# Performance work log

Hardware: AMD Instinct MI355X
Metric: run time of the kernel (lower is better)

Reference implementation:

```python
import jax, jax.numpy as jnp
import numpy as np

# Dims: N nodes, 2 CSR scales, hidden H=128, attention A=64, L=3 layers
N = 50000
E0, E1 = 600000, 200000   # edges per scale (avg degree 12 and 4)
H, A, L, S = 128, 64, 3, 2
F, CD = 16, 2             # field channels, coord dim
GEOM = S * (CD + 1)       # geometry embedding dim: mean rel offset + mean dist per scale


def setup_inputs() -> dict:
    key = jax.random.key(0)
    ks = jax.random.split(key, 12)
    coords = jax.random.normal(ks[0], (N, CD), jnp.float32)
    fields = jax.random.normal(ks[1], (N, F), jnp.float32)
    # CSR with fixed degrees (regular indptr, random irregular neighbor indices)
    indptr0 = (jnp.arange(N + 1, dtype=jnp.int32) * (E0 // N)).astype(jnp.int32)
    indices0 = jax.random.randint(ks[2], (E0,), 0, N, dtype=jnp.int32)
    indptr1 = (jnp.arange(N + 1, dtype=jnp.int32) * (E1 // N)).astype(jnp.int32)
    indices1 = jax.random.randint(ks[3], (E1,), 0, N, dtype=jnp.int32)
    # Learned parameters
    W_in = jax.random.normal(ks[4], (F + GEOM, H), jnp.float32) / np.sqrt(F + GEOM)
    b_in = jnp.zeros((H,), jnp.float32)
    Wq = jax.random.normal(ks[5], (L, S, H, A), jnp.float32) / np.sqrt(H)
    Wk = jax.random.normal(ks[6], (L, S, H, A), jnp.float32) / np.sqrt(H)
    Wv = jax.random.normal(ks[7], (L, S, H, H), jnp.float32) / np.sqrt(H)
    Wo = jax.random.normal(ks[8], (L, S * H, H), jnp.float32) / np.sqrt(S * H)
    bo = jnp.zeros((L, H), jnp.float32)
    return {"coords": coords, "fields": fields,
            "indptr0": indptr0, "indices0": indices0,
            "indptr1": indptr1, "indices1": indices1,
            "W_in": W_in, "b_in": b_in, "Wq": Wq, "Wk": Wk, "Wv": Wv,
            "Wo": Wo, "bo": bo}


def _csr_rows(indptr, num_edges):
    deg = indptr[1:] - indptr[:-1]
    return jnp.repeat(jnp.arange(indptr.shape[0] - 1), deg, total_repeat_length=num_edges)


def _geom_scale(coords, rows, cols, indptr):
    # per-node mean relative offset and mean neighbor distance over one scale
    n = indptr.shape[0] - 1
    rel = coords[cols] - coords[rows]                     # [E, CD]
    dist = jnp.linalg.norm(rel, axis=-1, keepdims=True)   # [E, 1]
    deg = (indptr[1:] - indptr[:-1]).astype(coords.dtype)[:, None]
    feats = jnp.concatenate([rel, dist], axis=-1)         # [E, CD+1]
    return jax.ops.segment_sum(feats, rows, num_segments=n) / jnp.maximum(deg, 1.0)


def _segment_softmax(scores, rows, n):
    m = jax.ops.segment_max(scores, rows, num_segments=n)
    ex = jnp.exp(scores - m[rows])
    den = jax.ops.segment_sum(ex, rows, num_segments=n)
    return ex / den[rows]


def reference(coords, fields, indptr0, indices0, indptr1, indices1,
              W_in, b_in, Wq, Wk, Wv, Wo, bo):
    n = coords.shape[0]
    csr = [(indptr0, indices0), (indptr1, indices1)]
    rows = [_csr_rows(ip, ix.shape[0]) for ip, ix in csr]
    # geometry embedding: concat per-scale neighborhood stats -> [N, GEOM]
    geom = jnp.concatenate(
        [_geom_scale(coords, rows[s], csr[s][1], csr[s][0]) for s in range(len(csr))], axis=-1)
    # prologue: concat fields+geom, Dense, gelu (flax gelu is tanh-approx)
    x = jax.nn.gelu(jnp.concatenate([fields, geom], axis=-1) @ W_in + b_in)
    eps = 1e-6
    for l in range(Wq.shape[0]):
        aggs = []
        for s in range(Wq.shape[1]):
            r, c = rows[s], csr[s][1]
            q = x @ Wq[l, s]           # [N, A]
            k = x @ Wk[l, s]           # [N, A]
            v = x @ Wv[l, s]           # [N, H]
            qn = q / (jnp.linalg.norm(q, axis=-1, keepdims=True) + eps)
            kn = k / (jnp.linalg.norm(k, axis=-1, keepdims=True) + eps)
            score = jnp.sum(qn[r] * kn[c], axis=-1)       # cosine attention per edge
            alpha = _segment_softmax(score, r, n)
            aggs.append(jax.ops.segment_sum(alpha[:, None] * v[c], r, num_segments=n))
        x = x + jax.nn.gelu(jnp.concatenate(aggs, axis=-1) @ Wo[l] + bo[l])
    return x
```

## Files before the change

kernel.cpp:

```cpp
#include <hip/hip_runtime.h>
#include <hip/hip_fp16.h>
#include <math.h>

#define HD 128

typedef _Float16 f16x8 __attribute__((ext_vector_type(8)));
typedef float f32x4 __attribute__((ext_vector_type(4)));

__device__ __forceinline__ f16x8 f16x8_zero() {
    f16x8 v = {(_Float16)0, (_Float16)0, (_Float16)0, (_Float16)0,
               (_Float16)0, (_Float16)0, (_Float16)0, (_Float16)0};
    return v;
}

__device__ __forceinline__ float gelu_tanh(float v) {
    float v3 = v * v * v;
    float t = tanhf(0.7978845608028654f * (v + 0.044715f * v3));
    return 0.5f * v * (1.0f + t);
}

__device__ __forceinline__ void store_h4(__half* p, float4 a) {
    __half2 lo = __float22half2_rn(make_float2(a.x, a.y));
    __half2 hi = __float22half2_rn(make_float2(a.z, a.w));
    uint2 u;
    u.x = *(unsigned*)&lo;
    u.y = *(unsigned*)&hi;
    *(uint2*)p = u;
}

__device__ __forceinline__ float4 load_h4(const __half* p) {
    uint2 raw = *(const uint2*)p;
    float2 lo = __half22float2(*(__half2*)&raw.x);
    float2 hi = __half22float2(*(__half2*)&raw.y);
    return make_float4(lo.x, lo.y, hi.x, hi.y);
}

__global__ void convert_wqkv_kernel(const float* __restrict__ Wq,
                                    const float* __restrict__ Wk,
                                    const float* __restrict__ Wv,
                                    __half* __restrict__ Wt) {
    int idx = blockIdx.x * 256 + threadIdx.x;
    if (idx >= 6 * 256 * 32) return;
    int ls = idx / (256 * 32);
    int rem = idx - ls * (256 * 32);
    int oc = rem >> 5;
    int k4 = rem & 31;
    const float* src;
    int stride, col;
    if (oc < 64)       { src = Wq + (size_t)ls * 128 * 64;  stride = 64;  col = oc; }
    else if (oc < 128) { src = Wk + (size_t)ls * 128 * 64;  stride = 64;  col = oc - 64; }
    else               { src = Wv + (size_t)ls * 128 * 128; stride = 128; col = oc - 128; }
    float4 v;
    v.x = src[(k4 * 4 + 0) * stride + col];
    v.y = src[(k4 * 4 + 1) * stride + col];
    v.z = src[(k4 * 4 + 2) * stride + col];
    v.w = src[(k4 * 4 + 3) * stride + col];
    store_h4(&Wt[(size_t)ls * 256 * 128 + (size_t)oc * 128 + k4 * 4], v);
}

__global__ void convert_wo_kernel(const float* __restrict__ Wo,
                                  __half* __restrict__ Wot) {
    int idx = blockIdx.x * 256 + threadIdx.x;
    if (idx >= 3 * 128 * 64) return;
    int l = idx / (128 * 64);
    int rem = idx - l * (128 * 64);
    int oc = rem >> 6;
    int k4 = rem & 63;
    const float* src = Wo + (size_t)l * 256 * 128;
    float4 v;
    v.x = src[(k4 * 4 + 0) * 128 + oc];
    v.y = src[(k4 * 4 + 1) * 128 + oc];
    v.z = src[(k4 * 4 + 2) * 128 + oc];
    v.w = src[(k4 * 4 + 3) * 128 + oc];
    store_h4(&Wot[(size_t)l * 128 * 256 + (size_t)oc * 256 + k4 * 4], v);
}

__global__ void geom_kernel(const float* __restrict__ coords,
                            const int* __restrict__ ip0, const int* __restrict__ ix0,
                            const int* __restrict__ ip1, const int* __restrict__ ix1,
                            float* __restrict__ geom, int n) {
    int i = blockIdx.x * blockDim.x + threadIdx.x;
    if (i >= n) return;
    float cx = coords[2 * i], cy = coords[2 * i + 1];
    #pragma unroll
    for (int s = 0; s < 2; ++s) {
        const int* ip = s ? ip1 : ip0;
        const int* ix = s ? ix1 : ix0;
        int st = ip[i], en = ip[i + 1];
        float sx = 0.f, sy = 0.f, sd = 0.f;
        for (int e = st; e < en; ++e) {
            int c = ix[e];
            float dx = coords[2 * c] - cx;
            float dy = coords[2 * c + 1] - cy;
            sx += dx; sy += dy;
            sd += sqrtf(dx * dx + dy * dy);
        }
        float inv = 1.0f / fmaxf((float)(en - st), 1.0f);
        geom[6 * i + 3 * s + 0] = sx * inv;
        geom[6 * i + 3 * s + 1] = sy * inv;
        geom[6 * i + 3 * s + 2] = sd * inv;
    }
}

__global__ void prologue_kernel(const float* __restrict__ fields,
                                const float* __restrict__ geom,
                                const float* __restrict__ W_in,
                                const float* __restrict__ b_in,
                                float* __restrict__ x,
                                __half* __restrict__ xh, int n) {
    int node = blockIdx.x * 2 + (threadIdx.x >> 7);
    int col = threadIdx.x & 127;
    if (node >= n) return;
    float acc = b_in[col];
    const float* f = fields + (size_t)node * 16;
    const float* g = geom + (size_t)node * 6;
    #pragma unroll
    for (int k = 0; k < 16; ++k) acc += f[k] * W_in[k * HD + col];
    #pragma unroll
    for (int k = 0; k < 6; ++k) acc += g[k] * W_in[(16 + k) * HD + col];
    float r = gelu_tanh(acc);
    x[(size_t)node * HD + col] = r;
    xh[(size_t)node * HD + col] = __float2half(r);
}

__global__ __launch_bounds__(256)
void qkv_mfma_kernel(const __half* __restrict__ xh,
                     const __half* __restrict__ Wt,
                     __half* __restrict__ qh,
                     __half* __restrict__ kh,
                     __half* __restrict__ vh,
                     int n) {
    __shared__ __half Xs[64 * 128];
    int t = threadIdx.x;
    int lane = t & 63, w = t >> 6;
    int m0 = blockIdx.x * 64;

    #pragma unroll
    for (int it = 0; it < 4; ++it) {
        int idx = t + it * 256;
        int row = idx >> 4, slot = idx & 15;
        int sw = slot ^ (row & 7);
        f16x8 v = f16x8_zero();
        if (m0 + row < n)
            v = *(const f16x8*)&xh[(size_t)(m0 + row) * 128 + slot * 8];
        *(f16x8*)&Xs[row * 128 + sw * 8] = v;
    }
    __syncthreads();

    int lr = lane & 15, lq = lane >> 4;
    f32x4 acc[4][4];
    #pragma unroll
    for (int nf = 0; nf < 4; ++nf)
        #pragma unroll
        for (int of = 0; of < 4; ++of) {
            f32x4 z = {0.f, 0.f, 0.f, 0.f};
            acc[nf][of] = z;
        }

    const __half* Wbase = Wt + (size_t)(w * 64) * 128;
    #pragma unroll
    for (int ts = 0; ts < 4; ++ts) {
        int koct = ts * 4 + lq;
        f16x8 wf[4], xf[4];
        #pragma unroll
        for (int of = 0; of < 4; ++of)
            wf[of] = *(const f16x8*)&Wbase[(size_t)(of * 16 + lr) * 128 + koct * 8];
        #pragma unroll
        for (int nf = 0; nf < 4; ++nf) {
            int row = nf * 16 + lr;
            int sw = koct ^ (row & 7);
            xf[nf] = *(const f16x8*)&Xs[row * 128 + sw * 8];
        }
        #pragma unroll
        for (int nf = 0; nf < 4; ++nf)
            #pragma unroll
            for (int of = 0; of < 4; ++of)
                acc[nf][of] = __builtin_amdgcn_mfma_f32_16x16x32_f16(
                    wf[of], xf[nf], acc[nf][of], 0, 0, 0);
    }

    if (w < 2) {
        #pragma unroll
        for (int nf = 0; nf < 4; ++nf) {
            float s = 0.f;
            #pragma unroll
            for (int of = 0; of < 4; ++of) {
                f32x4 a = acc[nf][of];
                s += a[0] * a[0] + a[1] * a[1] + a[2] * a[2] + a[3] * a[3];
            }
            s += __shfl_xor(s, 16, 64);
            s += __shfl_xor(s, 32, 64);
            float f = 1.0f / (sqrtf(s) + 1e-6f);
            #pragma unroll
            for (int of = 0; of < 4; ++of) {
                acc[nf][of][0] *= f; acc[nf][of][1] *= f;
                acc[nf][of][2] *= f; acc[nf][of][3] *= f;
            }
        }
    }

    #pragma unroll
    for (int nf = 0; nf < 4; ++nf) {
        int node = m0 + nf * 16 + lr;
        if (node >= n) continue;
        #pragma unroll
        for (int of = 0; of < 4; ++of) {
            int oc = of * 16 + lq * 4;
            float4 v = make_float4(acc[nf][of][0], acc[nf][of][1],
                                   acc[nf][of][2], acc[nf][of][3]);
            if (w == 0)      store_h4(&qh[(size_t)node * 64 + oc], v);
            else if (w == 1) store_h4(&kh[(size_t)node * 64 + oc], v);
            else if (w == 2) store_h4(&vh[(size_t)node * 128 + oc], v);
            else             store_h4(&vh[(size_t)node * 128 + 64 + oc], v);
        }
    }
}

template<int DEG>
__global__ void attn_kernel_t(const __half* __restrict__ qh,
                              const __half* __restrict__ kh,
                              const __half* __restrict__ vh,
                              const int* __restrict__ indptr,
                              const int* __restrict__ indices,
                              __half* __restrict__ aggh,
                              int scale, int n) {
    int wid = threadIdx.x >> 6;
    int lane = threadIdx.x & 63;
    int i = blockIdx.x * (blockDim.x >> 6) + wid;
    if (i >= n) return;
    int g = lane >> 4, sl = lane & 15;
    int st = indptr[i];

    float4 q = load_h4(&qh[(size_t)i * 64 + sl * 4]);

    float sc[DEG];
    constexpr int NIT = (DEG + 3) / 4;
    #pragma unroll
    for (int it = 0; it < NIT; ++it) {
        int e = it * 4 + g;
        int ee = (e < DEG) ? e : (DEG - 1);
        int c = indices[st + ee];
        float4 k = load_h4(&kh[(size_t)c * 64 + sl * 4]);
        float p = q.x * k.x + q.y * k.y + q.z * k.z + q.w * k.w;
        p += __shfl_xor(p, 1, 64);
        p += __shfl_xor(p, 2, 64);
        p += __shfl_xor(p, 4, 64);
        p += __shfl_xor(p, 8, 64);
        #pragma unroll
        for (int j = 0; j < 4; ++j) {
            int e2 = it * 4 + j;
            if (e2 < DEG) sc[e2] = __shfl(p, j * 16, 64);
        }
    }

    float mx = sc[0];
    #pragma unroll
    for (int e = 1; e < DEG; ++e) mx = fmaxf(mx, sc[e]);
    float den = 0.f;
    #pragma unroll
    for (int e = 0; e < DEG; ++e) { sc[e] = __expf(sc[e] - mx); den += sc[e]; }
    float inv = 1.0f / den;

    int half = lane >> 5, hl = lane & 31;
    float4 a = make_float4(0.f, 0.f, 0.f, 0.f);
    #pragma unroll
    for (int it = 0; it < DEG / 2; ++it) {
        int c = indices[st + 2 * it + half];
        float al = (half ? sc[2 * it + 1] : sc[2 * it]) * inv;
        float4 v = load_h4(&vh[(size_t)c * 128 + hl * 4]);
        a.x += al * v.x; a.y += al * v.y; a.z += al * v.z; a.w += al * v.w;
    }
    a.x += __shfl_xor(a.x, 32, 64);
    a.y += __shfl_xor(a.y, 32, 64);
    a.z += __shfl_xor(a.z, 32, 64);
    a.w += __shfl_xor(a.w, 32, 64);
    if (half == 0)
        store_h4(&aggh[(size_t)i * 256 + scale * 128 + hl * 4], a);
}

__global__ void attn_generic(const __half* __restrict__ qh,
                             const __half* __restrict__ kh,
                             const __half* __restrict__ vh,
                             const int* __restrict__ indptr,
                             const int* __restrict__ indices,
                             __half* __restrict__ aggh, int scale, int n) {
    int wid = threadIdx.x >> 6;
    int lane = threadIdx.x & 63;
    int i = blockIdx.x * (blockDim.x >> 6) + wid;
    if (i >= n) return;
    int g = lane >> 4, sl = lane & 15;
    int st = indptr[i];
    int deg = indptr[i + 1] - st;
    if (deg > 32) deg = 32;
    if (deg <= 0) {
        if (lane < 32)
            store_h4(&aggh[(size_t)i * 256 + scale * 128 + (lane & 31) * 4],
                     make_float4(0.f, 0.f, 0.f, 0.f));
        return;
    }
    float4 q = load_h4(&qh[(size_t)i * 64 + sl * 4]);
    float sc[32];
    for (int e0 = 0; e0 < deg; e0 += 4) {
        int e = e0 + g;
        int ee = (e < deg) ? e : (deg - 1);
        int c = indices[st + ee];
        float4 k = load_h4(&kh[(size_t)c * 64 + sl * 4]);
        float p = q.x * k.x + q.y * k.y + q.z * k.z + q.w * k.w;
        p += __shfl_xor(p, 1, 64);
        p += __shfl_xor(p, 2, 64);
        p += __shfl_xor(p, 4, 64);
        p += __shfl_xor(p, 8, 64);
        for (int j = 0; j < 4; ++j)
            if (e0 + j < deg) sc[e0 + j] = __shfl(p, j * 16, 64);
    }
    float mx = -INFINITY;
    for (int e = 0; e < deg; ++e) mx = fmaxf(mx, sc[e]);
    float den = 0.f;
    for (int e = 0; e < deg; ++e) { sc[e] = __expf(sc[e] - mx); den += sc[e]; }
    float inv = 1.0f / den;
    int half = lane >> 5, hl = lane & 31;
    float4 a = make_float4(0.f, 0.f, 0.f, 0.f);
    for (int e0 = 0; e0 < deg; e0 += 2) {
        int e = e0 + half;
        if (e < deg) {
            int c = indices[st + e];
            float al = sc[e] * inv;
            float4 v = load_h4(&vh[(size_t)c * 128 + hl * 4]);
            a.x += al * v.x; a.y += al * v.y; a.z += al * v.z; a.w += al * v.w;
        }
    }
    a.x += __shfl_xor(a.x, 32, 64);
    a.y += __shfl_xor(a.y, 32, 64);
    a.z += __shfl_xor(a.z, 32, 64);
    a.w += __shfl_xor(a.w, 32, 64);
    if (half == 0)
        store_h4(&aggh[(size_t)i * 256 + scale * 128 + hl * 4], a);
}

__global__ __launch_bounds__(256)
void wo_mfma_kernel(const __half* __restrict__ aggh,
                    const __half* __restrict__ Wot,
                    const float* __restrict__ bo,
                    float* __restrict__ x,
                    __half* __restrict__ xh,
                    int n) {
    __shared__ __half As[64 * 256];
    int t = threadIdx.x;
    int lane = t & 63, w = t >> 6;
    int m0 = blockIdx.x * 64;

    #pragma unroll
    for (int it = 0; it < 8; ++it) {
        int idx = t + it * 256;
        int row = idx >> 5, slot = idx & 31;
        int sw = slot ^ (row & 7);
        f16x8 v = f16x8_zero();
        if (m0 + row < n)
            v = *(const f16x8*)&aggh[(size_t)(m0 + row) * 256 + slot * 8];
        *(f16x8*)&As[row * 256 + sw * 8] = v;
    }
    __syncthreads();

    int lr = lane & 15, lq = lane >> 4;
    f32x4 acc[4][2];
    #pragma unroll
    for (int nf = 0; nf < 4; ++nf)
        #pragma unroll
        for (int of = 0; of < 2; ++of) {
            f32x4 z = {0.f, 0.f, 0.f, 0.f};
            acc[nf][of] = z;
        }

    const __half* Wbase = Wot + (size_t)(w * 32) * 256;
    #pragma unroll
    for (int ts = 0; ts < 8; ++ts) {
        int koct = ts * 4 + lq;
        f16x8 wf[2], af[4];
        #pragma unroll
        for (int of = 0; of < 2; ++of)
            wf[of] = *(const f16x8*)&Wbase[(size_t)(of * 16 + lr) * 256 + koct * 8];
        #pragma unroll
        for (int nf = 0; nf < 4; ++nf) {
            int row = nf * 16 + lr;
            int sw = koct ^ (row & 7);
            af[nf] = *(const f16x8*)&As[row * 256 + sw * 8];
        }
        #pragma unroll
        for (int nf = 0; nf < 4; ++nf)
            #pragma unroll
            for (int of = 0; of < 2; ++of)
                acc[nf][of] = __builtin_amdgcn_mfma_f32_16x16x32_f16(
                    wf[of], af[nf], acc[nf][of], 0, 0, 0);
    }

    #pragma unroll
    for (int nf = 0; nf < 4; ++nf) {
        int node = m0 + nf * 16 + lr;
        if (node >= n) continue;
        #pragma unroll
        for (int of = 0; of < 2; ++of) {
            int oc = w * 32 + of * 16 + lq * 4;
            float4 b = *(const float4*)&bo[oc];
            float4 xv = *(const float4*)&x[(size_t)node * 128 + oc];
            float4 r;
            r.x = xv.x + gelu_tanh(acc[nf][of][0] + b.x);
            r.y = xv.y + gelu_tanh(acc[nf][of][1] + b.y);
            r.z = xv.z + gelu_tanh(acc[nf][of][2] + b.z);
            r.w = xv.w + gelu_tanh(acc[nf][of][3] + b.w);
            *(float4*)&x[(size_t)node * 128 + oc] = r;
            store_h4(&xh[(size_t)node * 128 + oc], r);
        }
    }
}

extern "C" void kernel_launch(void* const* d_in, const int* in_sizes, int n_in,
                              void* d_out, int out_size, void* d_ws, size_t ws_size,
                              hipStream_t stream) {
    const float* coords = (const float*)d_in[0];
    const float* fields = (const float*)d_in[1];
    const int*   ip0    = (const int*)d_in[2];
    const int*   ix0    = (const int*)d_in[3];
    const int*   ip1    = (const int*)d_in[4];
    const int*   ix1    = (const int*)d_in[5];
    const float* W_in   = (const float*)d_in[6];
    const float* b_in   = (const float*)d_in[7];
    const float* Wq     = (const float*)d_in[8];
    const float* Wk     = (const float*)d_in[9];
    const float* Wv     = (const float*)d_in[10];
    const float* Wo     = (const float*)d_in[11];
    const float* bo     = (const float*)d_in[12];

    int n = in_sizes[0] / 2;
    float* x = (float*)d_out;

    char* ws = (char*)d_ws;
    size_t off = 0;
    auto carve = [&](size_t bytes) {
        void* p = ws + off;
        off = (off + bytes + 255) & ~(size_t)255;
        return p;
    };
    float*  geom = (float*)carve((size_t)n * 6 * 4);
    __half* xh   = (__half*)carve((size_t)n * 128 * 2);
    __half* qh   = (__half*)carve((size_t)n * 64 * 2);
    __half* kh   = (__half*)carve((size_t)n * 64 * 2);
    __half* vh   = (__half*)carve((size_t)n * 128 * 2);
    __half* aggh = (__half*)carve((size_t)n * 256 * 2);
    __half* Wt   = (__half*)carve((size_t)6 * 256 * 128 * 2);
    __half* Wot  = (__half*)carve((size_t)3 * 128 * 256 * 2);

    convert_wqkv_kernel<<<(6 * 256 * 32 + 255) / 256, 256, 0, stream>>>(Wq, Wk, Wv, Wt);
    convert_wo_kernel<<<(3 * 128 * 64 + 255) / 256, 256, 0, stream>>>(Wo, Wot);

    geom_kernel<<<(n + 255) / 256, 256, 0, stream>>>(coords, ip0, ix0, ip1, ix1, geom, n);
    prologue_kernel<<<(n + 1) / 2, 256, 0, stream>>>(fields, geom, W_in, b_in, x, xh, n);

    int deg0 = in_sizes[3] / n;
    int deg1 = in_sizes[5] / n;

    auto launch_attn = [&](int deg, const int* ip, const int* ix, int scale) {
        int ab = (n + 3) / 4;
        bool uniform = (deg * n == (scale ? in_sizes[5] : in_sizes[3]));
        if (uniform) {
            switch (deg) {
                case 4:  attn_kernel_t<4><<<ab, 256, 0, stream>>>(qh, kh, vh, ip, ix, aggh, scale, n); return;
                case 6:  attn_kernel_t<6><<<ab, 256, 0, stream>>>(qh, kh, vh, ip, ix, aggh, scale, n); return;
                case 8:  attn_kernel_t<8><<<ab, 256, 0, stream>>>(qh, kh, vh, ip, ix, aggh, scale, n); return;
                case 12: attn_kernel_t<12><<<ab, 256, 0, stream>>>(qh, kh, vh, ip, ix, aggh, scale, n); return;
                case 16: attn_kernel_t<16><<<ab, 256, 0, stream>>>(qh, kh, vh, ip, ix, aggh, scale, n); return;
            }
        }
        attn_generic<<<ab, 256, 0, stream>>>(qh, kh, vh, ip, ix, aggh, scale, n);
    };

    int gblocks = (n + 63) / 64;
    for (int l = 0; l < 3; ++l) {
        for (int s = 0; s < 2; ++s) {
            const __half* wt = Wt + (size_t)(l * 2 + s) * 256 * 128;
            qkv_mfma_kernel<<<gblocks, 256, 0, stream>>>(xh, wt, qh, kh, vh, n);
            launch_attn(s ? deg1 : deg0, s ? ip1 : ip0, s ? ix1 : ix0, s);
        }
        wo_mfma_kernel<<<gblocks, 256, 0, stream>>>(aggh, Wot + (size_t)l * 128 * 256,
                                                    bo + l * 128, x, xh, n);
    }
}
```

Measured before the change: 593.7 us.

## Fuse per-layer QKV for both scales and merge both scales' attention into one kernel

The geometry kernel is folded into the prologue kernel: one thread per node computes the neighbourhood stats into shared memory, and the geom buffer disappears. The QKV projection now computes both scales in a single 512-thread launch that reuses the staged X tile, writing into separate per-scale q/k/v buffers. A dual attention kernel processes both scales, with node/scale items interleaved across waves. Gathers of indices, K and V are batched into registers before use to raise memory-level parallelism. These changes cut kernel launches and the re-reading of x, at the cost of a serialized single-lane geom loop in the prologue and a dual path specialized to degrees 12 and 4.

After: 570.5 us. 1.04x faster.

```diff
diff --git a/kernel.cpp b/kernel.cpp
--- a/kernel.cpp
+++ b/kernel.cpp
@@ -75,69 +75,71 @@
     store_h4(&Wot[(size_t)l * 128 * 256 + (size_t)oc * 256 + k4 * 4], v);
 }
 
-__global__ void geom_kernel(const float* __restrict__ coords,
-                            const int* __restrict__ ip0, const int* __restrict__ ix0,
-                            const int* __restrict__ ip1, const int* __restrict__ ix1,
-                            float* __restrict__ geom, int n) {
-    int i = blockIdx.x * blockDim.x + threadIdx.x;
-    if (i >= n) return;
-    float cx = coords[2 * i], cy = coords[2 * i + 1];
-    #pragma unroll
-    for (int s = 0; s < 2; ++s) {
-        const int* ip = s ? ip1 : ip0;
-        const int* ix = s ? ix1 : ix0;
-        int st = ip[i], en = ip[i + 1];
-        float sx = 0.f, sy = 0.f, sd = 0.f;
-        for (int e = st; e < en; ++e) {
-            int c = ix[e];
-            float dx = coords[2 * c] - cx;
-            float dy = coords[2 * c + 1] - cy;
-            sx += dx; sy += dy;
-            sd += sqrtf(dx * dx + dy * dy);
-        }
-        float inv = 1.0f / fmaxf((float)(en - st), 1.0f);
-        geom[6 * i + 3 * s + 0] = sx * inv;
-        geom[6 * i + 3 * s + 1] = sy * inv;
-        geom[6 * i + 3 * s + 2] = sd * inv;
-    }
-}
-
-__global__ void prologue_kernel(const float* __restrict__ fields,
-                                const float* __restrict__ geom,
-                                const float* __restrict__ W_in,
-                                const float* __restrict__ b_in,
-                                float* __restrict__ x,
-                                __half* __restrict__ xh, int n) {
-    int node = blockIdx.x * 2 + (threadIdx.x >> 7);
+__global__ void geom_prologue_kernel(const float* __restrict__ coords,
+                                     const float* __restrict__ fields,
+                                     const int* __restrict__ ip0, const int* __restrict__ ix0,
+                                     const int* __restrict__ ip1, const int* __restrict__ ix1,
+                                     const float* __restrict__ W_in,
+                                     const float* __restrict__ b_in,
+                                     float* __restrict__ x,
+                                     __half* __restrict__ xh, int n) {
+    __shared__ float gsh[2][6];
+    int slot = threadIdx.x >> 7;
+    int node = blockIdx.x * 2 + slot;
     int col = threadIdx.x & 127;
-    if (node >= n) return;
+    bool valid = node < n;
+
+    if (valid && col == 0) {
+        float cx = coords[2 * node], cy = coords[2 * node + 1];
+        #pragma unroll
+        for (int s = 0; s < 2; ++s) {
+            const int* ip = s ? ip1 : ip0;
+            const int* ix = s ? ix1 : ix0;
+            int st = ip[node], en = ip[node + 1];
+            float sx = 0.f, sy = 0.f, sd = 0.f;
+            for (int e = st; e < en; ++e) {
+                int c = ix[e];
+                float dx = coords[2 * c] - cx;
+                float dy = coords[2 * c + 1] - cy;
+                sx += dx; sy += dy;
+                sd += sqrtf(dx * dx + dy * dy);
+            }
+            float inv = 1.0f / fmaxf((float)(en - st), 1.0f);
+            gsh[slot][3 * s + 0] = sx * inv;
+            gsh[slot][3 * s + 1] = sy * inv;
+            gsh[slot][3 * s + 2] = sd * inv;
+        }
+    }
+    __syncthreads();
+    if (!valid) return;
+
     float acc = b_in[col];
     const float* f = fields + (size_t)node * 16;
-    const float* g = geom + (size_t)node * 6;
     #pragma unroll
     for (int k = 0; k < 16; ++k) acc += f[k] * W_in[k * HD + col];
     #pragma unroll
-    for (int k = 0; k < 6; ++k) acc += g[k] * W_in[(16 + k) * HD + col];
+    for (int k = 0; k < 6; ++k) acc += gsh[slot][k] * W_in[(16 + k) * HD + col];
     float r = gelu_tanh(acc);
     x[(size_t)node * HD + col] = r;
     xh[(size_t)node * HD + col] = __float2half(r);
 }
 
-__global__ __launch_bounds__(256)
-void qkv_mfma_kernel(const __half* __restrict__ xh,
-                     const __half* __restrict__ Wt,
-                     __half* __restrict__ qh,
-                     __half* __restrict__ kh,
-                     __half* __restrict__ vh,
-                     int n) {
+__global__ __launch_bounds__(512)
+void qkv_dual_mfma_kernel(const __half* __restrict__ xh,
+                          const __half* __restrict__ WtL,
+                          __half* __restrict__ qh0, __half* __restrict__ kh0,
+                          __half* __restrict__ vh0,
+                          __half* __restrict__ qh1, __half* __restrict__ kh1,
+                          __half* __restrict__ vh1,
+                          int n) {
     __shared__ __half Xs[64 * 128];
     int t = threadIdx.x;
     int lane = t & 63, w = t >> 6;
     int m0 = blockIdx.x * 64;
 
     #pragma unroll
-    for (int it = 0; it < 4; ++it) {
-        int idx = t + it * 256;
+    for (int it = 0; it < 2; ++it) {
+        int idx = t + it * 512;
         int row = idx >> 4, slot = idx & 15;
         int sw = slot ^ (row & 7);
         f16x8 v = f16x8_zero();
@@ -147,6 +149,7 @@
     }
     __syncthreads();
 
+    int scale = w >> 2, sub = w & 3;
     int lr = lane & 15, lq = lane >> 4;
     f32x4 acc[4][4];
     #pragma unroll
@@ -157,7 +160,7 @@
             acc[nf][of] = z;
         }
 
-    const __half* Wbase = Wt + (size_t)(w * 64) * 128;
+    const __half* Wbase = WtL + ((size_t)scale * 256 + sub * 64) * 128;
     #pragma unroll
     for (int ts = 0; ts < 4; ++ts) {
         int koct = ts * 4 + lq;
@@ -179,7 +182,7 @@
                     wf[of], xf[nf], acc[nf][of], 0, 0, 0);
     }
 
-    if (w < 2) {
+    if (sub < 2) {
         #pragma unroll
         for (int nf = 0; nf < 4; ++nf) {
             float s = 0.f;
@@ -199,6 +202,9 @@
         }
     }
 
+    __half* qh = scale ? qh1 : qh0;
+    __half* kh = scale ? kh1 : kh0;
+    __half* vh = scale ? vh1 : vh0;
     #pragma unroll
     for (int nf = 0; nf < 4; ++nf) {
         int node = m0 + nf * 16 + lr;
@@ -208,11 +214,109 @@
             int oc = of * 16 + lq * 4;
             float4 v = make_float4(acc[nf][of][0], acc[nf][of][1],
                                    acc[nf][of][2], acc[nf][of][3]);
-            if (w == 0)      store_h4(&qh[(size_t)node * 64 + oc], v);
-            else if (w == 1) store_h4(&kh[(size_t)node * 64 + oc], v);
-            else if (w == 2) store_h4(&vh[(size_t)node * 128 + oc], v);
-            else             store_h4(&vh[(size_t)node * 128 + 64 + oc], v);
-        }
+            if (sub == 0)      store_h4(&qh[(size_t)node * 64 + oc], v);
+            else if (sub == 1) store_h4(&kh[(size_t)node * 64 + oc], v);
+            else if (sub == 2) store_h4(&vh[(size_t)node * 128 + oc], v);
+            else               store_h4(&vh[(size_t)node * 128 + 64 + oc], v);
+        }
+    }
+}
+
+template<int DEG>
+__device__ __forceinline__ void attn_one(const __half* __restrict__ qh,
+                                         const __half* __restrict__ kh,
+                                         const __half* __restrict__ vh,
+                                         const int* __restrict__ ixs,
+                                         __half* __restrict__ out,
+                                         int node, int lane) {
+    int g = lane >> 4, sl = lane & 15;
+    constexpr int NIT = (DEG + 3) / 4;
+
+    int cidx[NIT];
+    #pragma unroll
+    for (int it = 0; it < NIT; ++it) {
+        int e = it * 4 + g;
+        cidx[it] = ixs[(e < DEG) ? e : (DEG - 1)];
+    }
+    float4 q = load_h4(&qh[(size_t)node * 64 + sl * 4]);
+    uint2 kraw[NIT];
+    #pragma unroll
+    for (int it = 0; it < NIT; ++it)
+        kraw[it] = *(const uint2*)&kh[(size_t)cidx[it] * 64 + sl * 4];
+
+    float sc[DEG];
+    #pragma unroll
+    for (int it = 0; it < NIT; ++it) {
+        float2 lo = __half22float2(*(__half2*)&kraw[it].x);
+        float2 hi = __half22float2(*(__half2*)&kraw[it].y);
+        float p = q.x * lo.x + q.y * lo.y + q.z * hi.x + q.w * hi.y;
+        p += __shfl_xor(p, 1, 64);
+        p += __shfl_xor(p, 2, 64);
+        p += __shfl_xor(p, 4, 64);
+        p += __shfl_xor(p, 8, 64);
+        #pragma unroll
+        for (int j = 0; j < 4; ++j) {
+            int e2 = it * 4 + j;
+            if (e2 < DEG) sc[e2] = __shfl(p, j * 16, 64);
+        }
+    }
+
+    float mx = sc[0];
+    #pragma unroll
+    for (int e = 1; e < DEG; ++e) mx = fmaxf(mx, sc[e]);
+    float den = 0.f;
+    #pragma unroll
+    for (int e = 0; e < DEG; ++e) { sc[e] = __expf(sc[e] - mx); den += sc[e]; }
+    float inv = 1.0f / den;
+
+    int half = lane >> 5, hl = lane & 31;
+    constexpr int VIT = DEG / 2;
+    int vc[VIT];
+    #pragma unroll
+    for (int it = 0; it < VIT; ++it) vc[it] = ixs[2 * it + half];
+    uint2 vraw[VIT];
+    #pragma unroll
+    for (int it = 0; it < VIT; ++it)
+        vraw[it] = *(const uint2*)&vh[(size_t)vc[it] * 128 + hl * 4];
+
+    float4 a = make_float4(0.f, 0.f, 0.f, 0.f);
+    #pragma unroll
+    for (int it = 0; it < VIT; ++it) {
+        float al = (half ? sc[2 * it + 1] : sc[2 * it]) * inv;
+        float2 lo = __half22float2(*(__half2*)&vraw[it].x);
+        float2 hi = __half22float2(*(__half2*)&vraw[it].y);
+        a.x += al * lo.x; a.y += al * lo.y; a.z += al * hi.x; a.w += al * hi.y;
+    }
+    a.x += __shfl_xor(a.x, 32, 64);
+    a.y += __shfl_xor(a.y, 32, 64);
+    a.z += __shfl_xor(a.z, 32, 64);
+    a.w += __shfl_xor(a.w, 32, 64);
+    if (half == 0) store_h4(&out[hl * 4], a);
+}
+
+template<int DEG0, int DEG1>
+__global__ __launch_bounds__(512)
+void attn_dual_kernel(const __half* __restrict__ qh0, const __half* __restrict__ kh0,
+                      const __half* __restrict__ vh0,
+                      const __half* __restrict__ qh1, const __half* __restrict__ kh1,
+                      const __half* __restrict__ vh1,
+                      const int* __restrict__ ip0, const int* __restrict__ ix0,
+                      const int* __restrict__ ip1, const int* __restrict__ ix1,
+                      __half* __restrict__ aggh, int n) {
+    int wid = threadIdx.x >> 6;
+    int lane = threadIdx.x & 63;
+    long item = (long)blockIdx.x * 8 + wid;
+    if (item >= 2L * n) return;
+    int node = (int)(item >> 1);
+    int scale = (int)(item & 1);
+    if (scale == 0) {
+        int st = ip0[node];
+        attn_one<DEG0>(qh0, kh0, vh0, ix0 + st,
+                       aggh + (size_t)node * 256, node, lane);
+    } else {
+        int st = ip1[node];
+        attn_one<DEG1>(qh1, kh1, vh1, ix1 + st,
+                       aggh + (size_t)node * 256 + 128, node, lane);
     }
 }
 
@@ -222,60 +326,14 @@
                               const __half* __restrict__ vh,
                               const int* __restrict__ indptr,
                               const int* __restrict__ indices,
-                              __half* __restrict__ aggh,
-                              int scale, int n) {
+                              __half* __restrict__ aggh, int scale, int n) {
     int wid = threadIdx.x >> 6;
     int lane = threadIdx.x & 63;
     int i = blockIdx.x * (blockDim.x >> 6) + wid;
     if (i >= n) return;
-    int g = lane >> 4, sl = lane & 15;
     int st = indptr[i];
-
-    float4 q = load_h4(&qh[(size_t)i * 64 + sl * 4]);
-
-    float sc[DEG];
-    constexpr int NIT = (DEG + 3) / 4;
-    #pragma unroll
-    for (int it = 0; it < NIT; ++it) {
-        int e = it * 4 + g;
-        int ee = (e < DEG) ? e : (DEG - 1);
-        int c = indices[st + ee];
-        float4 k = load_h4(&kh[(size_t)c * 64 + sl * 4]);
-        float p = q.x * k.x + q.y * k.y + q.z * k.z + q.w * k.w;
-        p += __shfl_xor(p, 1, 64);
-        p += __shfl_xor(p, 2, 64);
-        p += __shfl_xor(p, 4, 64);
-        p += __shfl_xor(p, 8, 64);
-        #pragma unroll
-        for (int j = 0; j < 4; ++j) {
-            int e2 = it * 4 + j;
-            if (e2 < DEG) sc[e2] = __shfl(p, j * 16, 64);
-        }
-    }
-
-    float mx = sc[0];
-    #pragma unroll
-    for (int e = 1; e < DEG; ++e) mx = fmaxf(mx, sc[e]);
-    float den = 0.f;
-    #pragma unroll
-    for (int e = 0; e < DEG; ++e) { sc[e] = __expf(sc[e] - mx); den += sc[e]; }
-    float inv = 1.0f / den;
-
-    int half = lane >> 5, hl = lane & 31;
-    float4 a = make_float4(0.f, 0.f, 0.f, 0.f);
-    #pragma unroll
-    for (int it = 0; it < DEG / 2; ++it) {
-        int c = indices[st + 2 * it + half];
-        float al = (half ? sc[2 * it + 1] : sc[2 * it]) * inv;
-        float4 v = load_h4(&vh[(size_t)c * 128 + hl * 4]);
-        a.x += al * v.x; a.y += al * v.y; a.z += al * v.z; a.w += al * v.w;
-    }
-    a.x += __shfl_xor(a.x, 32, 64);
-    a.y += __shfl_xor(a.y, 32, 64);
-    a.z += __shfl_xor(a.z, 32, 64);
-    a.w += __shfl_xor(a.w, 32, 64);
-    if (half == 0)
-        store_h4(&aggh[(size_t)i * 256 + scale * 128 + hl * 4], a);
+    attn_one<DEG>(qh, kh, vh, indices + st,
+                  aggh + (size_t)i * 256 + scale * 128, i, lane);
 }
 
 __global__ void attn_generic(const __half* __restrict__ qh,
@@ -440,11 +498,13 @@
         off = (off + bytes + 255) & ~(size_t)255;
         return p;
     };
-    float*  geom = (float*)carve((size_t)n * 6 * 4);
     __half* xh   = (__half*)carve((size_t)n * 128 * 2);
-    __half* qh   = (__half*)carve((size_t)n * 64 * 2);
-    __half* kh   = (__half*)carve((size_t)n * 64 * 2);
-    __half* vh   = (__half*)carve((size_t)n * 128 * 2);
+    __half* qh0  = (__half*)carve((size_t)n * 64 * 2);
+    __half* kh0  = (__half*)carve((size_t)n * 64 * 2);
+    __half* vh0  = (__half*)carve((size_t)n * 128 * 2);
+    __half* qh1  = (__half*)carve((size_t)n * 64 * 2);
+    __half* kh1  = (__half*)carve((size_t)n * 64 * 2);
+    __half* vh1  = (__half*)carve((size_t)n * 128 * 2);
     __half* aggh = (__half*)carve((size_t)n * 256 * 2);
     __half* Wt   = (__half*)carve((size_t)6 * 256 * 128 * 2);
     __half* Wot  = (__half*)carve((size_t)3 * 128 * 256 * 2);
@@ -452,16 +512,20 @@
     convert_wqkv_kernel<<<(6 * 256 * 32 + 255) / 256, 256, 0, stream>>>(Wq, Wk, Wv, Wt);
     convert_wo_kernel<<<(3 * 128 * 64 + 255) / 256, 256, 0, stream>>>(Wo, Wot);
 
-    geom_kernel<<<(n + 255) / 256, 256, 0, stream>>>(coords, ip0, ix0, ip1, ix1, geom, n);
-    prologue_kernel<<<(n + 1) / 2, 256, 0, stream>>>(fields, geom, W_in, b_in, x, xh, n);
+    geom_prologue_kernel<<<(n + 1) / 2, 256, 0, stream>>>(coords, fields, ip0, ix0,
+                                                          ip1, ix1, W_in, b_in,
+                                                          x, xh, n);
 
     int deg0 = in_sizes[3] / n;
     int deg1 = in_sizes[5] / n;
-
-    auto launch_attn = [&](int deg, const int* ip, const int* ix, int scale) {
+    bool uni0 = (deg0 * n == in_sizes[3]);
+    bool uni1 = (deg1 * n == in_sizes[5]);
+
+    auto launch_attn_single = [&](int deg, bool uni, const int* ip, const int* ix,
+                                  const __half* qh, const __half* kh, const __half* vh,
+                                  int scale) {
         int ab = (n + 3) / 4;
-        bool uniform = (deg * n == (scale ? in_sizes[5] : in_sizes[3]));
-        if (uniform) {
+        if (uni) {
             switch (deg) {
                 case 4:  attn_kernel_t<4><<<ab, 256, 0, stream>>>(qh, kh, vh, ip, ix, aggh, scale, n); return;
                 case 6:  attn_kernel_t<6><<<ab, 256, 0, stream>>>(qh, kh, vh, ip, ix, aggh, scale, n); return;
@@ -473,12 +537,20 @@
         attn_generic<<<ab, 256, 0, stream>>>(qh, kh, vh, ip, ix, aggh, scale, n);
     };
 
+    bool dual_ok = uni0 && uni1 && deg0 == 12 && deg1 == 4;
+    int dual_blocks = (int)((2L * n + 7) / 8);
     int gblocks = (n + 63) / 64;
+
     for (int l = 0; l < 3; ++l) {
-        for (int s = 0; s < 2; ++s) {
-            const __half* wt = Wt + (size_t)(l * 2 + s) * 256 * 128;
-            qkv_mfma_kernel<<<gblocks, 256, 0, stream>>>(xh, wt, qh, kh, vh, n);
-            launch_attn(s ? deg1 : deg0, s ? ip1 : ip0, s ? ix1 : ix0, s);
+        const __half* WtL = Wt + (size_t)(l * 2) * 256 * 128;
+        qkv_dual_mfma_kernel<<<gblocks, 512, 0, stream>>>(xh, WtL, qh0, kh0, vh0,
+                                                          qh1, kh1, vh1, n);
+        if (dual_ok) {
+            attn_dual_kernel<12, 4><<<dual_blocks, 512, 0, stream>>>(
+                qh0, kh0, vh0, qh1, kh1, vh1, ip0, ix0, ip1, ix1, aggh, n);
+        } else {
+            launch_attn_single(deg0, uni0, ip0, ix0, qh0, kh0, vh0, 0);
+            launch_attn_single(deg1, uni1, ip1, ix1, qh1, kh1, vh1, 1);
         }
         wo_mfma_kernel<<<gblocks, 256, 0, stream>>>(aggh, Wot + (size_t)l * 128 * 256,
                                                     bo + l * 128, x, xh, n);
```
